# Kernel optimization log

Hardware: AMD Instinct MI355X
Metric: run time of the kernel (lower is better)

## Reference

```python
import jax, jax.numpy as jnp
import numpy as np

NEG_SLOPE = 0.2
N_NODES = 50000


def gat_conv(x, src, dst, W, a_src, a_dst, b, n_nodes):
    """One PyG-style GATConv layer (eval mode, self-loops already in src/dst).
    x: [N, F_in]; W: [F_in, H*C]; a_src/a_dst: [H, C]; b: [H*C] or [C].
    Returns per-node, per-head outputs [N, H, C].
    """
    H, C = a_src.shape
    h = (x @ W).reshape(-1, H, C)                      # [N, H, C]
    s_src = jnp.sum(h * a_src[None], axis=-1)          # [N, H]
    s_dst = jnp.sum(h * a_dst[None], axis=-1)          # [N, H]
    e = jax.nn.leaky_relu(s_src[src] + s_dst[dst], NEG_SLOPE)   # [E, H]
    # segment softmax over incoming edges of each destination node
    m = jax.ops.segment_max(e, dst, num_segments=n_nodes)       # [N, H]
    w = jnp.exp(e - m[dst])                                     # [E, H]
    denom = jax.ops.segment_sum(w, dst, num_segments=n_nodes)   # [N, H]
    alpha = w / denom[dst]                                      # [E, H]
    # weighted aggregation of source features
    out = jax.ops.segment_sum(alpha[:, :, None] * h[src], dst, num_segments=n_nodes)
    return out  # [N, H, C]


def setup_inputs() -> dict:
    key = jax.random.key(0)
    ks = jax.random.split(key, 12)
    N, F_in, Hid, H, F_out = N_NODES, 128, 64, 4, 128
    E = 800000
    x = jax.random.normal(ks[0], (N, F_in), dtype=jnp.float32)
    edge_index = jax.random.randint(ks[1], (2, E), 0, N, dtype=jnp.int64)
    sc = 0.1
    return {
        "x": x,
        "edge_index": edge_index,
        "W1": jax.random.normal(ks[2], (F_in, H * Hid), dtype=jnp.float32) * sc,
        "att_src1": jax.random.normal(ks[3], (H, Hid), dtype=jnp.float32) * sc,
        "att_dst1": jax.random.normal(ks[4], (H, Hid), dtype=jnp.float32) * sc,
        "b1": jnp.zeros((H * Hid,), dtype=jnp.float32),
        "W2": jax.random.normal(ks[5], (H * Hid, F_out), dtype=jnp.float32) * sc,
        "att_src2": jax.random.normal(ks[6], (1, F_out), dtype=jnp.float32) * sc,
        "att_dst2": jax.random.normal(ks[7], (1, F_out), dtype=jnp.float32) * sc,
        "b2": jnp.zeros((F_out,), dtype=jnp.float32),
    }


def reference(x, edge_index, W1, att_src1, att_dst1, b1, W2, att_src2, att_dst2, b2):
    N = x.shape[0]
    # PyG GATConv adds self-loops by default
    loops = jnp.arange(N, dtype=edge_index.dtype)
    src = jnp.concatenate([edge_index[0], loops])
    dst = jnp.concatenate([edge_index[1], loops])
    # layer 1: heads=4, concat -> [N, H*Hid], then ELU (dropout is identity in eval)
    h1 = gat_conv(x, src, dst, W1, att_src1, att_dst1, b1, N)    # [N, H, Hid]
    h1 = h1.reshape(N, -1) + b1
    h1 = jax.nn.elu(h1)
    # layer 2: heads=1, concat=False -> mean over the single head
    h2 = gat_conv(h1, src, dst, W2, att_src2, att_dst2, b2, N)   # [N, 1, F_out]
    out = h2[:, 0, :] + b2
    return out
```

## Files before the change

### kernel.cpp

```cpp
#include <hip/hip_runtime.h>
#include <cmath>

typedef __attribute__((ext_vector_type(8))) short bf16x8;
typedef __attribute__((ext_vector_type(4))) float f32x4;

static __device__ __forceinline__ unsigned short f2bf(float f) {
    unsigned u = __float_as_uint(f);
    unsigned r = (u + 0x7fffu + ((u >> 16) & 1u)) >> 16;
    return (unsigned short)r;
}
static __device__ __forceinline__ unsigned packbf(float a, float b) {
    return (unsigned)f2bf(a) | ((unsigned)f2bf(b) << 16);
}
static __device__ __forceinline__ float bflo(unsigned u) { return __uint_as_float(u << 16); }
static __device__ __forceinline__ float bfhi(unsigned u) { return __uint_as_float(u & 0xffff0000u); }

__global__ void prep_k(const float* __restrict__ x, const float* __restrict__ W1,
                       const float* __restrict__ W2, const int* __restrict__ dst,
                       unsigned* __restrict__ xb,
                       unsigned short* __restrict__ Wt1, unsigned short* __restrict__ Wt2,
                       int* __restrict__ deg, int NX2, int NW1, int NW2, int E) {
    int i = blockIdx.x * blockDim.x + threadIdx.x;
    if (i < NX2) {
        float2 v = reinterpret_cast<const float2*>(x)[i];
        xb[i] = packbf(v.x, v.y);
        return;
    }
    i -= NX2;
    if (i < NW1) { int nn = i / 128, k = i % 128; Wt1[i] = f2bf(W1[(size_t)k * 256 + nn]); return; }
    i -= NW1;
    if (i < NW2) { int nn = i / 256, k = i % 256; Wt2[i] = f2bf(W2[(size_t)k * 128 + nn]); return; }
    i -= NW2;
    if (i < E) atomicAdd(&deg[dst[i]], 1);
}

#define SCAN_BLK 256
#define SCAN_ELEMS 2048

__global__ void scan1_k(const int* __restrict__ deg, int* __restrict__ rowstart,
                        int* __restrict__ bsums, int N) {
    __shared__ int sh[SCAN_BLK];
    int t = threadIdx.x;
    int base = blockIdx.x * SCAN_ELEMS + t * 8;
    int vals[8];
    int sum = 0;
#pragma unroll
    for (int i = 0; i < 8; ++i) {
        int idx = base + i;
        vals[i] = (idx < N) ? (deg[idx] + 1) : 0;
        sum += vals[i];
    }
    sh[t] = sum;
    __syncthreads();
    for (int off = 1; off < SCAN_BLK; off <<= 1) {
        int v = (t >= off) ? sh[t - off] : 0;
        __syncthreads();
        sh[t] += v;
        __syncthreads();
    }
    int run = sh[t] - sum;
    if (t == SCAN_BLK - 1) bsums[blockIdx.x] = sh[t];
#pragma unroll
    for (int i = 0; i < 8; ++i) {
        int idx = base + i;
        if (idx < N) rowstart[idx] = run;
        run += vals[i];
    }
}
__global__ void scan2_k(int* __restrict__ bsums, int nb) {
    int lane = threadIdx.x;
    int own = (lane < nb) ? bsums[lane] : 0;
    int v = own;
    for (int off = 1; off < 64; off <<= 1) {
        int t = __shfl_up(v, off, 64);
        if (lane >= off) v += t;
    }
    if (lane < nb) bsums[lane] = v - own;
}
__global__ void scan3_init_k(int* __restrict__ rowstart, const int* __restrict__ bsums,
                             int* __restrict__ adj, int* __restrict__ cursor, int N, int total) {
    int i = blockIdx.x * blockDim.x + threadIdx.x;
    if (i < N) {
        int r = rowstart[i] + bsums[i / SCAN_ELEMS];
        rowstart[i] = r;
        adj[r] = i;
        cursor[i] = r + 1;
    } else if (i == N) {
        rowstart[N] = total;
    }
}
__global__ void scatter_k(const int* __restrict__ src, const int* __restrict__ dst, int E,
                          int* __restrict__ cursor, int* __restrict__ adj) {
    int e = blockIdx.x * blockDim.x + threadIdx.x;
    if (e >= E) return;
    int pos = atomicAdd(&cursor[dst[e]], 1);
    adj[pos] = src[e];
}

template<int K, int NOUT>
__global__ __launch_bounds__(256) void gemm_mfma_k(const unsigned* __restrict__ Ab,
                                                   const unsigned* __restrict__ Bt,
                                                   unsigned short* __restrict__ Yb, int N) {
    __shared__ unsigned short As[128 * 64];
    __shared__ unsigned short Bs[64 * 64];
    int tid = threadIdx.x;
    int lane = tid & 63, wid = tid >> 6;
    int wm = wid >> 1, wc = wid & 1;
    int m0 = blockIdx.x * 128;
    int n0 = blockIdx.y * 64;

    f32x4 acc[4][2] = {};

    for (int k0 = 0; k0 < K; k0 += 64) {
#pragma unroll
        for (int p = 0; p < 4; ++p) {
            int gl = p * 256 + tid;
            int row = gl >> 3, g = gl & 7;
            int grow = m0 + row; if (grow >= N) grow = N - 1;
            uint4 v = *reinterpret_cast<const uint4*>(Ab + (size_t)grow * (K / 2) + k0 / 2 + g * 4);
            *reinterpret_cast<uint4*>((char*)As + row * 128 + ((g ^ (row & 7)) << 4)) = v;
        }
#pragma unroll
        for (int p = 0; p < 2; ++p) {
            int gl = p * 256 + tid;
            int row = gl >> 3, g = gl & 7;
            uint4 v = *reinterpret_cast<const uint4*>(Bt + (size_t)(n0 + row) * (K / 2) + k0 / 2 + g * 4);
            *reinterpret_cast<uint4*>((char*)Bs + row * 128 + ((g ^ (row & 7)) << 4)) = v;
        }
        __syncthreads();

        bf16x8 bfrag[2][2];
#pragma unroll
        for (int kk = 0; kk < 2; ++kk)
#pragma unroll
            for (int no = 0; no < 2; ++no) {
                int row = wc * 32 + no * 16 + (lane & 15);
                int g = kk * 4 + (lane >> 4);
                bfrag[kk][no] = *reinterpret_cast<const bf16x8*>((char*)Bs + row * 128 + ((g ^ (row & 7)) << 4));
            }
#pragma unroll
        for (int mo = 0; mo < 4; ++mo) {
#pragma unroll
            for (int kk = 0; kk < 2; ++kk) {
                int row = wm * 64 + mo * 16 + (lane & 15);
                int g = kk * 4 + (lane >> 4);
                bf16x8 afrag = *reinterpret_cast<const bf16x8*>((char*)As + row * 128 + ((g ^ (row & 7)) << 4));
                acc[mo][0] = __builtin_amdgcn_mfma_f32_16x16x32_bf16(afrag, bfrag[kk][0], acc[mo][0], 0, 0, 0);
                acc[mo][1] = __builtin_amdgcn_mfma_f32_16x16x32_bf16(afrag, bfrag[kk][1], acc[mo][1], 0, 0, 0);
            }
        }
        __syncthreads();
    }
#pragma unroll
    for (int mo = 0; mo < 4; ++mo)
#pragma unroll
        for (int no = 0; no < 2; ++no) {
            int col = n0 + wc * 32 + no * 16 + (lane & 15);
            int rbase = m0 + wm * 64 + mo * 16 + (lane >> 4) * 4;
#pragma unroll
            for (int j = 0; j < 4; ++j) {
                int row = rbase + j;
                if (row < N) Yb[(size_t)row * NOUT + col] = f2bf(acc[mo][no][j]);
            }
        }
}

template<int H, int C>
__global__ void score_b_k(const unsigned* __restrict__ hb, const float* __restrict__ a_src,
                          const float* __restrict__ a_dst,
                          float* __restrict__ ssrc, float* __restrict__ sdst, int N) {
    int idx = blockIdx.x * blockDim.x + threadIdx.x;
    if (idx >= N * H) return;
    int n = idx / H, hh = idx % H;
    const uint4* hp = reinterpret_cast<const uint4*>(hb + (size_t)n * (H * C / 2) + hh * (C / 2));
    const float* as = a_src + hh * C;
    const float* ad = a_dst + hh * C;
    float ss = 0.f, sd = 0.f;
#pragma unroll
    for (int i = 0; i < C / 8; ++i) {
        uint4 u = hp[i];
        float v[8] = {bflo(u.x), bfhi(u.x), bflo(u.y), bfhi(u.y),
                      bflo(u.z), bfhi(u.z), bflo(u.w), bfhi(u.w)};
#pragma unroll
        for (int j = 0; j < 8; ++j) { ss += v[j] * as[i * 8 + j]; sd += v[j] * ad[i * 8 + j]; }
    }
    ssrc[idx] = ss;
    sdst[idx] = sd;
}

template<int H, int C, int GRP, bool ELU, bool OUT_BF16>
__global__ void node_agg_k(const int* __restrict__ rowstart, const int* __restrict__ adj,
                           const float* __restrict__ ssrc, const float* __restrict__ sdst,
                           const unsigned* __restrict__ hb, const float* __restrict__ bias,
                           void* __restrict__ outp, int N) {
    constexpr int HC = H * C;
    constexpr int ROW_U = HC / 2;
    constexpr int ULN = ROW_U / GRP;
    constexpr int FPLn = ULN * 2;
    constexpr int NG = 64 / GRP;
    constexpr int NGB = 4 * NG;
    int lane = threadIdx.x & 63;
    int w = threadIdx.x >> 6;
    int g = lane / GRP, ln = lane % GRP;
    int gid = w * NG + g;
    int n = blockIdx.x * NGB + gid;
    if (n >= N) return;

    __shared__ int   s_tab[NGB][64];
    __shared__ float a_tab[NGB][64 * H];

    int r0 = rowstart[n], r1 = rowstart[n + 1];
    int deg = r1 - r0;

    float sd[H];
#pragma unroll
    for (int h = 0; h < H; ++h) sd[h] = sdst[n * H + h];

    int hA = (ln * FPLn) / C;
    const unsigned* hbl = hb + ln * ULN;
    float acc[FPLn];
#pragma unroll
    for (int f = 0; f < FPLn; ++f) acc[f] = 0.f;
    float l[H];
#pragma unroll
    for (int h = 0; h < H; ++h) l[h] = 0.f;

    if (deg <= 64) {
        for (int base = 0; base < deg; base += GRP) {
            int idx = base + ln;
            bool on = idx < deg;
            int s = adj[r0 + (on ? idx : 0)];
            float v[H];
            if constexpr (H == 4) {
                float4 sv = reinterpret_cast<const float4*>(ssrc)[s];
                v[0] = sv.x; v[1] = sv.y; v[2] = sv.z; v[3] = sv.w;
            } else {
                v[0] = ssrc[s];
            }
#pragma unroll
            for (int h = 0; h < H; ++h) {
                float t = v[h] + sd[h];
                t = t > 0.f ? t : 0.2f * t;
                float av = on ? __expf(t) : 0.f;
                l[h] += av;
                if (on) a_tab[gid][idx * H + h] = av;
            }
            if (on) s_tab[gid][idx] = s;
        }
#pragma unroll
        for (int off = GRP / 2; off; off >>= 1)
#pragma unroll
            for (int h = 0; h < H; ++h) l[h] += __shfl_xor(l[h], off, 64);

        int j = 0;
        for (; j + 3 < deg; j += 4) {
            int s0 = s_tab[gid][j],     s1 = s_tab[gid][j + 1];
            int s2 = s_tab[gid][j + 2], s3 = s_tab[gid][j + 3];
            float a0 = a_tab[gid][j * H + hA],       a1 = a_tab[gid][(j + 1) * H + hA];
            float a2 = a_tab[gid][(j + 2) * H + hA], a3 = a_tab[gid][(j + 3) * H + hA];
            uint4 u0 = *reinterpret_cast<const uint4*>(hbl + (size_t)s0 * ROW_U);
            uint4 u1 = *reinterpret_cast<const uint4*>(hbl + (size_t)s1 * ROW_U);
            uint4 u2 = *reinterpret_cast<const uint4*>(hbl + (size_t)s2 * ROW_U);
            uint4 u3 = *reinterpret_cast<const uint4*>(hbl + (size_t)s3 * ROW_U);
            acc[0] += a0 * bflo(u0.x); acc[1] += a0 * bfhi(u0.x);
            acc[2] += a0 * bflo(u0.y); acc[3] += a0 * bfhi(u0.y);
            acc[4] += a0 * bflo(u0.z); acc[5] += a0 * bfhi(u0.z);
            acc[6] += a0 * bflo(u0.w); acc[7] += a0 * bfhi(u0.w);
            acc[0] += a1 * bflo(u1.x); acc[1] += a1 * bfhi(u1.x);
            acc[2] += a1 * bflo(u1.y); acc[3] += a1 * bfhi(u1.y);
            acc[4] += a1 * bflo(u1.z); acc[5] += a1 * bfhi(u1.z);
            acc[6] += a1 * bflo(u1.w); acc[7] += a1 * bfhi(u1.w);
            acc[0] += a2 * bflo(u2.x); acc[1] += a2 * bfhi(u2.x);
            acc[2] += a2 * bflo(u2.y); acc[3] += a2 * bfhi(u2.y);
            acc[4] += a2 * bflo(u2.z); acc[5] += a2 * bfhi(u2.z);
            acc[6] += a2 * bflo(u2.w); acc[7] += a2 * bfhi(u2.w);
            acc[0] += a3 * bflo(u3.x); acc[1] += a3 * bfhi(u3.x);
            acc[2] += a3 * bflo(u3.y); acc[3] += a3 * bfhi(u3.y);
            acc[4] += a3 * bflo(u3.z); acc[5] += a3 * bfhi(u3.z);
            acc[6] += a3 * bflo(u3.w); acc[7] += a3 * bfhi(u3.w);
        }
        for (; j < deg; ++j) {
            int sj = s_tab[gid][j];
            float al = a_tab[gid][j * H + hA];
            uint4 u = *reinterpret_cast<const uint4*>(hbl + (size_t)sj * ROW_U);
            acc[0] += al * bflo(u.x); acc[1] += al * bfhi(u.x);
            acc[2] += al * bflo(u.y); acc[3] += al * bfhi(u.y);
            acc[4] += al * bflo(u.z); acc[5] += al * bfhi(u.z);
            acc[6] += al * bflo(u.w); acc[7] += al * bfhi(u.w);
        }
    } else {
        for (int e = r0 + ln; e < r1; e += GRP) {
            int s = adj[e];
#pragma unroll
            for (int h = 0; h < H; ++h) {
                float t = ssrc[s * H + h] + sd[h];
                t = t > 0.f ? t : 0.2f * t;
                l[h] += __expf(t);
            }
        }
#pragma unroll
        for (int off = GRP / 2; off; off >>= 1)
#pragma unroll
            for (int h = 0; h < H; ++h) l[h] += __shfl_xor(l[h], off, 64);
        float sdh = sd[hA];
        for (int e = r0; e < r1; ++e) {
            int s = adj[e];
            float t = ssrc[s * H + hA] + sdh;
            t = t > 0.f ? t : 0.2f * t;
            float al = __expf(t);
            uint4 u = *reinterpret_cast<const uint4*>(hbl + (size_t)s * ROW_U);
            acc[0] += al * bflo(u.x); acc[1] += al * bfhi(u.x);
            acc[2] += al * bflo(u.y); acc[3] += al * bfhi(u.y);
            acc[4] += al * bflo(u.z); acc[5] += al * bfhi(u.z);
            acc[6] += al * bflo(u.w); acc[7] += al * bfhi(u.w);
        }
    }

    float invl = __builtin_amdgcn_rcpf(l[hA]);
#pragma unroll
    for (int f = 0; f < FPLn; ++f) {
        float v = acc[f] * invl + bias[ln * FPLn + f];
        if (ELU) v = v > 0.f ? v : (__expf(v) - 1.f);
        acc[f] = v;
    }
    if constexpr (OUT_BF16) {
        unsigned* op = (unsigned*)outp + (size_t)n * ROW_U + ln * ULN;
        uint4 u = {packbf(acc[0], acc[1]), packbf(acc[2], acc[3]),
                   packbf(acc[4], acc[5]), packbf(acc[6], acc[7])};
        *reinterpret_cast<uint4*>(op) = u;
    } else {
        float* op = (float*)outp + (size_t)n * HC + ln * FPLn;
        *reinterpret_cast<float4*>(op) = make_float4(acc[0], acc[1], acc[2], acc[3]);
        *reinterpret_cast<float4*>(op + 4) = make_float4(acc[4], acc[5], acc[6], acc[7]);
    }
}

extern "C" void kernel_launch(void* const* d_in, const int* in_sizes, int n_in,
                              void* d_out, int out_size, void* d_ws, size_t ws_size,
                              hipStream_t stream) {
    const float* x   = (const float*)d_in[0];
    const int*   ei  = (const int*)d_in[1];
    const float* W1  = (const float*)d_in[2];
    const float* as1 = (const float*)d_in[3];
    const float* ad1 = (const float*)d_in[4];
    const float* b1  = (const float*)d_in[5];
    const float* W2  = (const float*)d_in[6];
    const float* as2 = (const float*)d_in[7];
    const float* ad2 = (const float*)d_in[8];
    const float* b2  = (const float*)d_in[9];
    float* out = (float*)d_out;

    const int N  = in_sizes[0] / 128;
    const int E  = in_sizes[1] / 2;
    const int ET = E + N;
    const int* src = ei;
    const int* dst = ei + E;

    unsigned* ws = (unsigned*)d_ws;
    unsigned* xb    = ws;
    unsigned* h1b   = xb    + (size_t)N * 64;
    unsigned* agg1b = h1b   + (size_t)N * 128;
    unsigned* h2b   = agg1b + (size_t)N * 128;
    unsigned* Wt1   = h2b   + (size_t)N * 64;
    unsigned* Wt2   = Wt1   + 16384;
    float*    ssrc1 = (float*)(Wt2 + 16384);
    float*    sdst1 = ssrc1 + (size_t)N * 4;
    float*    ssrc2 = sdst1 + (size_t)N * 4;
    float*    sdst2 = ssrc2 + N;
    int*      deg   = (int*)(sdst2 + N);
    int*      rowst = deg + N;
    int*      bsums = rowst + N + 1;
    int*      adj   = bsums + 64;

    const int B = 256;
    auto blocks = [](size_t n, int b) { return (int)((n + b - 1) / b); };
    const int nscan = (N + SCAN_ELEMS - 1) / SCAN_ELEMS;

    hipMemsetAsync(deg, 0, (size_t)N * 4, stream);
    {
        int NX2 = N * 64, NW1 = 128 * 256, NW2 = 256 * 128;
        size_t tot = (size_t)NX2 + NW1 + NW2 + E;
        prep_k<<<blocks(tot, B), B, 0, stream>>>(x, W1, W2, dst, xb, (unsigned short*)Wt1,
                                                 (unsigned short*)Wt2, deg, NX2, NW1, NW2, E);
    }

    scan1_k<<<nscan, SCAN_BLK, 0, stream>>>(deg, rowst, bsums, N);
    scan2_k<<<1, 64, 0, stream>>>(bsums, nscan);
    scan3_init_k<<<blocks(N + 1, B), B, 0, stream>>>(rowst, bsums, adj, deg, N, ET);
    scatter_k<<<blocks(E, B), B, 0, stream>>>(src, dst, E, deg, adj);

    {
        dim3 g((N + 127) / 128, 256 / 64);
        gemm_mfma_k<128, 256><<<g, 256, 0, stream>>>(xb, (const unsigned*)Wt1, (unsigned short*)h1b, N);
    }
    score_b_k<4, 64><<<blocks((size_t)N * 4, B), B, 0, stream>>>(h1b, as1, ad1, ssrc1, sdst1, N);
    node_agg_k<4, 64, 32, true, true><<<(N + 7) / 8, 256, 0, stream>>>(rowst, adj, ssrc1, sdst1, h1b, b1, agg1b, N);

    {
        dim3 g((N + 127) / 128, 128 / 64);
        gemm_mfma_k<256, 128><<<g, 256, 0, stream>>>(agg1b, (const unsigned*)Wt2, (unsigned short*)h2b, N);
    }
    score_b_k<1, 128><<<blocks(N, B), B, 0, stream>>>(h2b, as2, ad2, ssrc2, sdst2, N);
    node_agg_k<1, 128, 16, false, false><<<(N + 15) / 16, 256, 0, stream>>>(rowst, adj, ssrc2, sdst2, h2b, b2, out, N);
}
```

Before: 255.2 us.

## Fuse attention score computation into the MFMA GEMM epilogue

After: 244.8 us. -4.0%, faster.

```diff
diff --git a/kernel.cpp b/kernel.cpp
--- a/kernel.cpp
+++ b/kernel.cpp
@@ -97,12 +97,17 @@
     adj[pos] = src[e];
 }
 
-template<int K, int NOUT>
-__global__ __launch_bounds__(256) void gemm_mfma_k(const unsigned* __restrict__ Ab,
-                                                   const unsigned* __restrict__ Bt,
-                                                   unsigned short* __restrict__ Yb, int N) {
+template<int K, int NOUT, int H, int C>
+__global__ __launch_bounds__(256) void gemm_score_k(const unsigned* __restrict__ Ab,
+                                                    const unsigned* __restrict__ Bt,
+                                                    unsigned short* __restrict__ Yb,
+                                                    const float* __restrict__ asrc,
+                                                    const float* __restrict__ adst,
+                                                    float* __restrict__ ssrc,
+                                                    float* __restrict__ sdst, int N) {
     __shared__ unsigned short As[128 * 64];
     __shared__ unsigned short Bs[64 * 64];
+    __shared__ float sred[2][2][128];
     int tid = threadIdx.x;
     int lane = tid & 63, wid = tid >> 6;
     int wm = wid >> 1, wc = wid & 1;
@@ -151,6 +156,7 @@
         }
         __syncthreads();
     }
+
 #pragma unroll
     for (int mo = 0; mo < 4; ++mo)
 #pragma unroll
@@ -163,29 +169,53 @@
                 if (row < N) Yb[(size_t)row * NOUT + col] = f2bf(acc[mo][no][j]);
             }
         }
-}
-
-template<int H, int C>
-__global__ void score_b_k(const unsigned* __restrict__ hb, const float* __restrict__ a_src,
-                          const float* __restrict__ a_dst,
-                          float* __restrict__ ssrc, float* __restrict__ sdst, int N) {
-    int idx = blockIdx.x * blockDim.x + threadIdx.x;
-    if (idx >= N * H) return;
-    int n = idx / H, hh = idx % H;
-    const uint4* hp = reinterpret_cast<const uint4*>(hb + (size_t)n * (H * C / 2) + hh * (C / 2));
-    const float* as = a_src + hh * C;
-    const float* ad = a_dst + hh * C;
-    float ss = 0.f, sd = 0.f;
-#pragma unroll
-    for (int i = 0; i < C / 8; ++i) {
-        uint4 u = hp[i];
-        float v[8] = {bflo(u.x), bfhi(u.x), bflo(u.y), bfhi(u.y),
-                      bflo(u.z), bfhi(u.z), bflo(u.w), bfhi(u.w)};
-#pragma unroll
-        for (int j = 0; j < 8; ++j) { ss += v[j] * as[i * 8 + j]; sd += v[j] * ad[i * 8 + j]; }
-    }
-    ssrc[idx] = ss;
-    sdst[idx] = sd;
+
+    float cs0, cs1, cd0, cd1;
+    {
+        int c0 = n0 + wc * 32 + (lane & 15);
+        cs0 = asrc[c0]; cd0 = adst[c0];
+        cs1 = asrc[c0 + 16]; cd1 = adst[c0 + 16];
+    }
+#pragma unroll
+    for (int mo = 0; mo < 4; ++mo) {
+        float ps[4], pd[4];
+#pragma unroll
+        for (int j = 0; j < 4; ++j) {
+            ps[j] = acc[mo][0][j] * cs0 + acc[mo][1][j] * cs1;
+            pd[j] = acc[mo][0][j] * cd0 + acc[mo][1][j] * cd1;
+        }
+#pragma unroll
+        for (int off = 8; off; off >>= 1)
+#pragma unroll
+            for (int j = 0; j < 4; ++j) {
+                ps[j] += __shfl_xor(ps[j], off, 64);
+                pd[j] += __shfl_xor(pd[j], off, 64);
+            }
+        if ((lane & 15) == 0) {
+            int rl = wm * 64 + mo * 16 + (lane >> 4) * 4;
+#pragma unroll
+            for (int j = 0; j < 4; ++j) {
+                sred[wc][0][rl + j] = ps[j];
+                sred[wc][1][rl + j] = pd[j];
+            }
+        }
+    }
+    __syncthreads();
+    if (tid < 128) {
+        int grow = m0 + tid;
+        if (grow < N) {
+            float fs = sred[0][0][tid] + sred[1][0][tid];
+            float fd = sred[0][1][tid] + sred[1][1][tid];
+            if constexpr (C <= 64) {
+                int hh = n0 / C;
+                ssrc[(size_t)grow * H + hh] = fs;
+                sdst[(size_t)grow * H + hh] = fd;
+            } else {
+                atomicAdd(&ssrc[grow], fs);
+                atomicAdd(&sdst[grow], fd);
+            }
+        }
+    }
 }
 
 template<int H, int C, int GRP, bool ELU, bool OUT_BF16>
@@ -376,7 +406,7 @@
     auto blocks = [](size_t n, int b) { return (int)((n + b - 1) / b); };
     const int nscan = (N + SCAN_ELEMS - 1) / SCAN_ELEMS;
 
-    hipMemsetAsync(deg, 0, (size_t)N * 4, stream);
+    hipMemsetAsync(ssrc2, 0, (size_t)N * 3 * 4, stream);
     {
         int NX2 = N * 64, NW1 = 128 * 256, NW2 = 256 * 128;
         size_t tot = (size_t)NX2 + NW1 + NW2 + E;
@@ -391,15 +421,15 @@
 
     {
         dim3 g((N + 127) / 128, 256 / 64);
-        gemm_mfma_k<128, 256><<<g, 256, 0, stream>>>(xb, (const unsigned*)Wt1, (unsigned short*)h1b, N);
-    }
-    score_b_k<4, 64><<<blocks((size_t)N * 4, B), B, 0, stream>>>(h1b, as1, ad1, ssrc1, sdst1, N);
+        gemm_score_k<128, 256, 4, 64><<<g, 256, 0, stream>>>(
+            xb, (const unsigned*)Wt1, (unsigned short*)h1b, as1, ad1, ssrc1, sdst1, N);
+    }
     node_agg_k<4, 64, 32, true, true><<<(N + 7) / 8, 256, 0, stream>>>(rowst, adj, ssrc1, sdst1, h1b, b1, agg1b, N);
 
     {
         dim3 g((N + 127) / 128, 128 / 64);
-        gemm_mfma_k<256, 128><<<g, 256, 0, stream>>>(agg1b, (const unsigned*)Wt2, (unsigned short*)h2b, N);
-    }
-    score_b_k<1, 128><<<blocks(N, B), B, 0, stream>>>(h2b, as2, ad2, ssrc2, sdst2, N);
+        gemm_score_k<256, 128, 1, 128><<<g, 256, 0, stream>>>(
+            agg1b, (const unsigned*)Wt2, (unsigned short*)h2b, as2, ad2, ssrc2, sdst2, N);
+    }
     node_agg_k<1, 128, 16, false, false><<<(N + 15) / 16, 256, 0, stream>>>(rowst, adj, ssrc2, sdst2, h2b, b2, out, N);
 }
```
